# Kernel tuning notes

Hardware: AMD Instinct MI355X
Metric: run time of the kernel (lower is better)

## Reference

```python
import jax, jax.numpy as jnp
import numpy as np
import math

B, S, D_MODEL, H = 4, 256, 2048, 256
HEAD_DIM = D_MODEL // H  # 8


def setup_inputs() -> dict:
    key = jax.random.key(0)
    ks = jax.random.split(key, 10)
    w_scale = 0.02
    inp = {
        "x": jax.random.normal(ks[0], (B, S, D_MODEL), dtype=jnp.float32),
        "phase_shift": jax.random.normal(ks[1], (H, 1, 1), dtype=jnp.float32),
        "Wq": jax.random.normal(ks[2], (D_MODEL, D_MODEL), dtype=jnp.float32) * w_scale,
        "bq": jnp.zeros((D_MODEL,), dtype=jnp.float32),
        "Wk": jax.random.normal(ks[3], (D_MODEL, D_MODEL), dtype=jnp.float32) * w_scale,
        "bk": jnp.zeros((D_MODEL,), dtype=jnp.float32),
        "Wv": jax.random.normal(ks[4], (D_MODEL, D_MODEL), dtype=jnp.float32) * w_scale,
        "bv": jnp.zeros((D_MODEL,), dtype=jnp.float32),
        "Wo": jax.random.normal(ks[5], (D_MODEL, D_MODEL), dtype=jnp.float32) * w_scale,
        "bo": jnp.zeros((D_MODEL,), dtype=jnp.float32),
    }
    return inp


def _forward(x, phase_shift, Wq, bq, Wk, bk, Wv, bv, Wo, bo):
    b, s, dm = x.shape
    h = phase_shift.shape[0]
    d = dm // h
    # projections (torch Linear with random weights; stored as [in,out])
    q = (x @ Wq + bq).reshape(b, s, h, d)
    k = (x @ Wk + bk).reshape(b, s, h, d)
    v = (x @ Wv + bv).reshape(b, s, h, d)
    # complex phase rotation: q *= exp(+i phi), k *= exp(-i phi)
    # phase_shift (h,1,1) broadcasts against (b,s,h,d) -> varies along the s dim (requires s==h)
    c = jnp.cos(phase_shift)  # (h,1,1)
    sn = jnp.sin(phase_shift)
    qr, qi = q * c, q * sn          # Re/Im of rotated q
    kr, ki = k * c, -(k * sn)       # Re/Im of rotated k
    scale = 1.0 / math.sqrt(d)
    # per-(b,s) head-mixing scores: [b,s,h,h], complex matmul split into real/imag
    sr = (jnp.einsum('bshd,bsgd->bshg', qr, kr)
          - jnp.einsum('bshd,bsgd->bshg', qi, ki)) * scale
    si = (jnp.einsum('bshd,bsgd->bshg', qr, ki)
          + jnp.einsum('bshd,bsgd->bshg', qi, kr)) * scale  # analytically 0 (phases cancel)
    attn_r = jax.nn.softmax(sr, axis=-1)
    attn_i = jax.nn.softmax(si, axis=-1)  # faithful dual softmax; v is real so only
    # Re(attention @ v) = attn_r @ v reaches the output (.real is taken before o_proj)
    del attn_i
    out = jnp.einsum('bshg,bsgd->bshd', attn_r, v).reshape(b, s, dm)
    return out @ Wo + bo


def reference(x, phase_shift, Wq, bq, Wk, bk, Wv, bv, Wo, bo):
    return _forward(x, phase_shift, Wq, bq, Wk, bk, Wv, bv, Wo, bo)
```

## Files before the change

### kernel.cpp

```cpp
#include <hip/hip_runtime.h>
#include <math.h>

#define M_TOK 1024
#define DM    2048
#define NH    256
#define HD    8
#define SCALE 0.35355339059327373f

typedef _Float16 f16x8 __attribute__((ext_vector_type(8)));
typedef _Float16 f16x4 __attribute__((ext_vector_type(4)));
typedef float    f32x4 __attribute__((ext_vector_type(4)));

__global__ __launch_bounds__(256) void prep(
    const float* __restrict__ x, _Float16* __restrict__ xh,
    const float* __restrict__ W0, const float* __restrict__ W1,
    const float* __restrict__ W2, const float* __restrict__ W3,
    _Float16* __restrict__ T0, _Float16* __restrict__ T1,
    _Float16* __restrict__ T2, _Float16* __restrict__ T3)
{
    __shared__ float t[64][65];
    const int tid = threadIdx.x;
    const int z   = blockIdx.z;

    if (z == 4) {
        const int i = (blockIdx.y * 32 + blockIdx.x) * 256 + tid;
        const float4 a = ((const float4*)x)[2 * i];
        const float4 b = ((const float4*)x)[2 * i + 1];
        f16x8 v;
        v[0] = (_Float16)a.x; v[1] = (_Float16)a.y; v[2] = (_Float16)a.z; v[3] = (_Float16)a.w;
        v[4] = (_Float16)b.x; v[5] = (_Float16)b.y; v[6] = (_Float16)b.z; v[7] = (_Float16)b.w;
        ((f16x8*)xh)[i] = v;
        return;
    }

    const float* W = (z == 0) ? W0 : (z == 1) ? W1 : (z == 2) ? W2 : W3;
    _Float16*    T = (z == 0) ? T0 : (z == 1) ? T1 : (z == 2) ? T2 : T3;

    const int nb = blockIdx.x * 64;
    const int kb = blockIdx.y * 64;
    const int tr = tid >> 4;
    const int tc = (tid & 15) << 2;

    #pragma unroll
    for (int rr = 0; rr < 4; ++rr) {
        const int k = kb + rr * 16 + tr;
        const float4 v = *(const float4*)&W[(size_t)k * DM + nb + tc];
        t[rr * 16 + tr][tc + 0] = v.x;
        t[rr * 16 + tr][tc + 1] = v.y;
        t[rr * 16 + tr][tc + 2] = v.z;
        t[rr * 16 + tr][tc + 3] = v.w;
    }
    __syncthreads();
    #pragma unroll
    for (int rr = 0; rr < 4; ++rr) {
        const int n = nb + rr * 16 + tr;
        f16x4 v;
        #pragma unroll
        for (int j = 0; j < 4; ++j)
            v[j] = (_Float16)t[tc + j][rr * 16 + tr];
        *(f16x4*)&T[(size_t)n * DM + kb + tc] = v;
    }
}

template<int WGR, int WGC, int WTR, int WTC, bool F16OUT>
__global__ __launch_bounds__(256, 3) void gemm_db(
    const _Float16* __restrict__ A,
    const _Float16* __restrict__ Bt0, const float* __restrict__ b0, void* __restrict__ C0,
    const _Float16* __restrict__ Bt1, const float* __restrict__ b1, void* __restrict__ C1,
    const _Float16* __restrict__ Bt2, const float* __restrict__ b2, void* __restrict__ C2)
{
    constexpr int BM  = WGR * WTR * 16;
    constexpr int BN  = WGC * WTC * 16;
    static_assert(BN == 128, "col tile must be 128");
    constexpr int NA  = BM / 8;
    constexpr int NB  = 16;
    constexpr int NC  = NA + NB;
    constexpr int CPW = NC / 4;
    static_assert(NC % 4 == 0);
    constexpr int BUF = (BM + 128) * 64;

    __shared__ _Float16 smem[2 * BUF];

    const int which = blockIdx.x >> 4;
    const int bn    = (blockIdx.x & 15) * 128;
    const int bm    = blockIdx.y * BM;

    const _Float16* Bt   = (which == 0) ? Bt0 : (which == 1) ? Bt1 : Bt2;
    const float*    bias = (which == 0) ? b0  : (which == 1) ? b1  : b2;
    void*           C    = (which == 0) ? C0  : (which == 1) ? C1  : C2;

    const int tid  = threadIdx.x;
    const int lane = tid & 63;
    const int wv   = tid >> 6;
    const int wr   = (wv / WGC) * (WTR * 16);
    const int wc   = (wv % WGC) * (WTC * 16);
    const int lr   = lane & 15;
    const int lk   = lane >> 4;
    const int rx   = lr & 7;

    const _Float16* gsrc[CPW];
    int             loff[CPW];
    #pragma unroll
    for (int p = 0; p < CPW; ++p) {
        const int c   = wv * CPW + p;
        const int kch = ((lane & 7) ^ (lane >> 3)) << 3;
        if (c < NA) {
            const int rl = c * 8 + (lane >> 3);
            gsrc[p] = A + (size_t)(bm + rl) * DM + kch;
            loff[p] = c * 512 + lane * 8;
        } else {
            const int rl = (c - NA) * 8 + (lane >> 3);
            gsrc[p] = Bt + (size_t)(bn + rl) * DM + kch;
            loff[p] = BM * 64 + (c - NA) * 512 + lane * 8;
        }
    }

    int offA[WTR][2], offB[WTC][2];
    #pragma unroll
    for (int ks = 0; ks < 2; ++ks) {
        const int sw = (((ks << 2) | lk) ^ rx) << 3;
        #pragma unroll
        for (int i = 0; i < WTR; ++i)
            offA[i][ks] = (wr + i * 16 + lr) * 64 + sw;
        #pragma unroll
        for (int j = 0; j < WTC; ++j)
            offB[j][ks] = BM * 64 + (wc + j * 16 + lr) * 64 + sw;
    }

    f32x4 acc[WTR][WTC] = {};

    auto prefetch = [&](int buf) {
        #pragma unroll
        for (int p = 0; p < CPW; ++p) {
            __builtin_amdgcn_global_load_lds(
                (const __attribute__((address_space(1))) void*)gsrc[p],
                (__attribute__((address_space(3))) void*)(smem + buf * BUF + loff[p]),
                16, 0, 0);
            gsrc[p] += 64;
        }
    };

    auto compute = [&](int buf) {
        const _Float16* base = smem + buf * BUF;
        #pragma unroll
        for (int ks = 0; ks < 2; ++ks) {
            f16x8 aF[WTR], bF[WTC];
            #pragma unroll
            for (int i = 0; i < WTR; ++i)
                aF[i] = *(const f16x8*)&base[offA[i][ks]];
            #pragma unroll
            for (int j = 0; j < WTC; ++j)
                bF[j] = *(const f16x8*)&base[offB[j][ks]];
            #pragma unroll
            for (int i = 0; i < WTR; ++i)
                #pragma unroll
                for (int j = 0; j < WTC; ++j)
                    acc[i][j] = __builtin_amdgcn_mfma_f32_16x16x32_f16(aF[i], bF[j], acc[i][j], 0, 0, 0);
        }
    };

    prefetch(0);
    #pragma unroll 1
    for (int it2 = 0; it2 < 16; ++it2) {
        __syncthreads();
        prefetch(1);
        compute(0);
        __syncthreads();
        if (it2 < 15) prefetch(0);
        compute(1);
    }

    #pragma unroll
    for (int i = 0; i < WTR; ++i) {
        #pragma unroll
        for (int j = 0; j < WTC; ++j) {
            const int col = bn + wc + j * 16 + lr;
            const float bv = bias[col];
            #pragma unroll
            for (int r = 0; r < 4; ++r) {
                const int row = bm + wr + i * 16 + lk * 4 + r;
                const float v = acc[i][j][r] + bv;
                if (F16OUT)
                    ((_Float16*)C)[(size_t)row * DM + col] = (_Float16)v;
                else
                    ((float*)C)[(size_t)row * DM + col] = v;
            }
        }
    }
}

__global__ __launch_bounds__(256) void attn_mfma(
    const _Float16* __restrict__ Qh, const _Float16* __restrict__ Kh,
    const _Float16* __restrict__ Vh, _Float16* __restrict__ Oh)
{
    __shared__ _Float16 Vt[8][264];
    __shared__ _Float16 Al[256][72];
    __shared__ _Float16 Ot[256][8];

    const int t    = blockIdx.x;
    const int tid  = threadIdx.x;
    const int lane = tid & 63;
    const int wv   = tid >> 6;
    const int col  = lane & 15;
    const int quad = lane >> 4;
    const int hbase = wv * 64;

    const _Float16* qb = Qh + (size_t)t * DM;
    const _Float16* kb = Kh + (size_t)t * DM;
    const _Float16* vb = Vh + (size_t)t * DM;

    {
        const f16x8 v = *(const f16x8*)(vb + tid * 8);
        #pragma unroll
        for (int d = 0; d < 8; ++d) Vt[d][tid] = v[d];
    }

    f16x8 qf[4];
    #pragma unroll
    for (int ht = 0; ht < 4; ++ht) {
        f16x8 v = {};
        if (quad == 0)
            v = *(const f16x8*)(qb + (hbase + ht * 16 + col) * 8);
        #pragma unroll
        for (int j = 0; j < 8; ++j) qf[ht][j] = v[j] * (_Float16)SCALE;
    }

    __syncthreads();

    const f32x4 zf = {};
    float rsum[4] = {};
    f32x4 oacc[4] = {};

    #pragma unroll 1
    for (int c = 0; c < 4; ++c) {
        const int gchunk = c * 64;

        f16x8 kf[4];
        #pragma unroll
        for (int gt = 0; gt < 4; ++gt) {
            f16x8 v = {};
            if (quad == 0)
                v = *(const f16x8*)(kb + (gchunk + gt * 16 + col) * 8);
            kf[gt] = v;
        }

        f32x4 s[4][4];
        #pragma unroll
        for (int gt = 0; gt < 4; ++gt)
            #pragma unroll
            for (int ht = 0; ht < 4; ++ht)
                s[gt][ht] = __builtin_amdgcn_mfma_f32_16x16x32_f16(kf[gt], qf[ht], zf, 0, 0, 0);

        #pragma unroll
        for (int gt = 0; gt < 4; ++gt) {
            #pragma unroll
            for (int ht = 0; ht < 4; ++ht) {
                f16x4 e4;
                #pragma unroll
                for (int r = 0; r < 4; ++r) {
                    e4[r] = (_Float16)__expf(s[gt][ht][r]);
                    rsum[ht] += (float)e4[r];
                }
                *(f16x4*)&Al[hbase + ht * 16 + col][gt * 16 + quad * 4] = e4;
            }
        }

        #pragma unroll
        for (int ks = 0; ks < 2; ++ks) {
            f16x8 vf = {};
            if (col < 8)
                vf = *(const f16x8*)&Vt[col][gchunk + ks * 32 + quad * 8];
            #pragma unroll
            for (int ht = 0; ht < 4; ++ht) {
                const f16x8 af = *(const f16x8*)&Al[hbase + ht * 16 + col][ks * 32 + quad * 8];
                oacc[ht] = __builtin_amdgcn_mfma_f32_16x16x32_f16(af, vf, oacc[ht], 0, 0, 0);
            }
        }
    }

    #pragma unroll
    for (int ht = 0; ht < 4; ++ht) {
        rsum[ht] += __shfl_xor(rsum[ht], 16, 64);
        rsum[ht] += __shfl_xor(rsum[ht], 32, 64);
    }

    #pragma unroll
    for (int ht = 0; ht < 4; ++ht) {
        #pragma unroll
        for (int r = 0; r < 4; ++r) {
            const float sh = __shfl(rsum[ht], quad * 4 + r, 64);
            const float v  = oacc[ht][r] / sh;
            if (col < 8)
                Ot[hbase + ht * 16 + quad * 4 + r][col] = (_Float16)v;
        }
    }
    const f16x8 ov = *(const f16x8*)&Ot[tid][0];
    *(f16x8*)(Oh + (size_t)t * DM + tid * 8) = ov;
}

extern "C" void kernel_launch(void* const* d_in, const int* in_sizes, int n_in,
                              void* d_out, int out_size, void* d_ws, size_t ws_size,
                              hipStream_t stream)
{
    const float* x  = (const float*)d_in[0];
    const float* Wq = (const float*)d_in[2];
    const float* bq = (const float*)d_in[3];
    const float* Wk = (const float*)d_in[4];
    const float* bk = (const float*)d_in[5];
    const float* Wv = (const float*)d_in[6];
    const float* bv = (const float*)d_in[7];
    const float* Wo = (const float*)d_in[8];
    const float* bo = (const float*)d_in[9];
    float* out = (float*)d_out;

    char* ws = (char*)d_ws;
    _Float16* xh  = (_Float16*)(ws);
    _Float16* Wtq = (_Float16*)(ws + (4u  << 20));
    _Float16* Wtk = (_Float16*)(ws + (12u << 20));
    _Float16* Wtv = (_Float16*)(ws + (20u << 20));
    _Float16* Wto = (_Float16*)(ws + (28u << 20));
    _Float16* Qh  = (_Float16*)(ws + (36u << 20));
    _Float16* Kh  = (_Float16*)(ws + (40u << 20));
    _Float16* Vh  = (_Float16*)(ws + (44u << 20));
    _Float16* Oh  = (_Float16*)(ws + (48u << 20));

    prep<<<dim3(32, 32, 5), dim3(256), 0, stream>>>(
        x, xh, Wq, Wk, Wv, Wo, Wtq, Wtk, Wtv, Wto);

    gemm_db<2, 2, 2, 4, true><<<dim3(48, 16), dim3(256), 0, stream>>>(xh,
        Wtq, bq, (void*)Qh,
        Wtk, bk, (void*)Kh,
        Wtv, bv, (void*)Vh);

    attn_mfma<<<dim3(M_TOK), dim3(256), 0, stream>>>(Qh, Kh, Vh, Oh);

    gemm_db<1, 4, 2, 2, false><<<dim3(16, 32), dim3(256), 0, stream>>>(Oh,
        Wto, bo, (void*)out,
        Wto, bo, (void*)out,
        Wto, bo, (void*)out);
}
```

Baseline: 201.1 us.

## Replace QKV projection GEMM with 32x32 MFMA kernel using direct-to-LDS loads

Adds a new QKV GEMM kernel with 128x128 tiles that uses 32x32x16 f16 MFMA instructions. The B operand is staged through swizzled LDS with global_load_lds, double-buffered, while A fragments are loaded straight from global into registers. The goal is to raise MFMA efficiency and cut LDS traffic for A, which matters more than before since the grid drops from 768 to 384 blocks. The trade-offs are lower occupancy (launch bounds of 2), heavier register pressure, and an epilogue that stores scalar f16 values without coalescing.

```diff
diff --git a/kernel.cpp b/kernel.cpp
--- a/kernel.cpp
+++ b/kernel.cpp
@@ -10,6 +10,7 @@
 typedef _Float16 f16x8 __attribute__((ext_vector_type(8)));
 typedef _Float16 f16x4 __attribute__((ext_vector_type(4)));
 typedef float    f32x4 __attribute__((ext_vector_type(4)));
+typedef float    f32x16 __attribute__((ext_vector_type(16)));
 
 __global__ __launch_bounds__(256) void prep(
     const float* __restrict__ x, _Float16* __restrict__ xh,
@@ -59,6 +60,115 @@
         for (int j = 0; j < 4; ++j)
             v[j] = (_Float16)t[tc + j][rr * 16 + tr];
         *(f16x4*)&T[(size_t)n * DM + kb + tc] = v;
+    }
+}
+
+__global__ __launch_bounds__(256, 2) void gemm_qkv32(
+    const _Float16* __restrict__ A,
+    const _Float16* __restrict__ Bt0, const float* __restrict__ b0, _Float16* __restrict__ C0,
+    const _Float16* __restrict__ Bt1, const float* __restrict__ b1, _Float16* __restrict__ C1,
+    const _Float16* __restrict__ Bt2, const float* __restrict__ b2, _Float16* __restrict__ C2)
+{
+    __shared__ _Float16 Bs[2][128 * 64];
+
+    const int which = blockIdx.x >> 4;
+    const int bn    = (blockIdx.x & 15) * 128;
+    const int bm    = blockIdx.y * 128;
+
+    const _Float16* Bt   = (which == 0) ? Bt0 : (which == 1) ? Bt1 : Bt2;
+    const float*    bias = (which == 0) ? b0  : (which == 1) ? b1  : b2;
+    _Float16*       C    = (which == 0) ? C0  : (which == 1) ? C1  : C2;
+
+    const int tid  = threadIdx.x;
+    const int lane = tid & 63;
+    const int wv   = tid >> 6;
+    const int wrow = wv >> 1;
+    const int wcol = wv & 1;
+    const int l31  = lane & 31;
+    const int lk   = lane >> 5;
+
+    const _Float16* gB[4];
+    int             lB[4];
+    #pragma unroll
+    for (int p = 0; p < 4; ++p) {
+        const int r = wv * 32 + p * 8 + (lane >> 3);
+        const int c = (lane & 7) ^ ((lane >> 3) & 7);
+        gB[p] = Bt + (size_t)(bn + r) * DM + c * 8;
+        lB[p] = (wv * 4 + p) * 512 + lane * 8;
+    }
+
+    const _Float16* pA[2];
+    #pragma unroll
+    for (int mt = 0; mt < 2; ++mt)
+        pA[mt] = A + (size_t)(bm + wrow * 64 + mt * 32 + l31) * DM + lk * 8;
+
+    f32x16 acc[2][2] = {};
+    f16x8  aR[2][2][4];
+
+    auto stageB = [&](int buf) {
+        #pragma unroll
+        for (int p = 0; p < 4; ++p) {
+            __builtin_amdgcn_global_load_lds(
+                (const __attribute__((address_space(1))) void*)gB[p],
+                (__attribute__((address_space(3))) void*)&Bs[buf][lB[p]], 16, 0, 0);
+            gB[p] += 64;
+        }
+    };
+    auto loadA = [&](int rb, int k0) {
+        #pragma unroll
+        for (int mt = 0; mt < 2; ++mt)
+            #pragma unroll
+            for (int ks = 0; ks < 4; ++ks)
+                aR[rb][mt][ks] = *(const f16x8*)(pA[mt] + k0 + ks * 16);
+    };
+    auto compute = [&](int buf, int rb) {
+        #pragma unroll
+        for (int ks = 0; ks < 4; ++ks) {
+            f16x8 bF[2];
+            #pragma unroll
+            for (int nt = 0; nt < 2; ++nt) {
+                const int n = wcol * 64 + nt * 32 + l31;
+                const int c = ks * 2 + lk;
+                bF[nt] = *(const f16x8*)&Bs[buf][n * 64 + (c ^ (n & 7)) * 8];
+            }
+            #pragma unroll
+            for (int mt = 0; mt < 2; ++mt)
+                #pragma unroll
+                for (int nt = 0; nt < 2; ++nt)
+                    acc[mt][nt] = __builtin_amdgcn_mfma_f32_32x32x16_f16(
+                        aR[rb][mt][ks], bF[nt], acc[mt][nt], 0, 0, 0);
+        }
+    };
+
+    stageB(0);
+    loadA(0, 0);
+    #pragma unroll 1
+    for (int it2 = 0; it2 < 16; ++it2) {
+        __syncthreads();
+        stageB(1);
+        loadA(1, (2 * it2 + 1) * 64);
+        compute(0, 0);
+        __syncthreads();
+        if (it2 < 15) {
+            stageB(0);
+            loadA(0, (2 * it2 + 2) * 64);
+        }
+        compute(1, 1);
+    }
+
+    #pragma unroll
+    for (int mt = 0; mt < 2; ++mt) {
+        #pragma unroll
+        for (int nt = 0; nt < 2; ++nt) {
+            const int col = bn + wcol * 64 + nt * 32 + l31;
+            const float bv = bias[col];
+            const int rbase = bm + wrow * 64 + mt * 32 + 4 * lk;
+            #pragma unroll
+            for (int r = 0; r < 16; ++r) {
+                const int row = rbase + (r & 3) + 8 * (r >> 2);
+                C[(size_t)row * DM + col] = (_Float16)(acc[mt][nt][r] + bv);
+            }
+        }
     }
 }
 
@@ -327,10 +437,10 @@
     prep<<<dim3(32, 32, 5), dim3(256), 0, stream>>>(
         x, xh, Wq, Wk, Wv, Wo, Wtq, Wtk, Wtv, Wto);
 
-    gemm_db<2, 2, 2, 4, true><<<dim3(48, 16), dim3(256), 0, stream>>>(xh,
-        Wtq, bq, (void*)Qh,
-        Wtk, bk, (void*)Kh,
-        Wtv, bv, (void*)Vh);
+    gemm_qkv32<<<dim3(48, 8), dim3(256), 0, stream>>>(xh,
+        Wtq, bq, Qh,
+        Wtk, bk, Kh,
+        Wtv, bv, Vh);
 
     attn_mfma<<<dim3(M_TOK), dim3(256), 0, stream>>>(Qh, Kh, Vh, Oh);
 
```

Result: slower. 242.3 us (+20.5%).
